# Performance work log

Measured on AMD Instinct MI355X. Metric: run time of the kernel, lower is better.

Reference implementation:

```python
import jax, jax.numpy as jnp
import numpy as np

MAX_SEQ = 512
HIDDEN = 1024
E = 2 * HIDDEN  # expansion
S = 128         # head dim s
EPS = 1e-5


def setup_inputs() -> dict:
    key = jax.random.key(0)
    ks = jax.random.split(key, 10)
    B, N = 32, 512
    x = jax.random.normal(ks[0], (B, N, HIDDEN), dtype=jnp.float32)
    attention_mask = jnp.ones((B, N), dtype=jnp.float32)
    gamma = jax.random.uniform(ks[1], (2, S), dtype=jnp.float32)
    beta = jax.random.uniform(ks[2], (2, S), dtype=jnp.float32)
    w = jax.random.uniform(ks[3], (2 * MAX_SEQ - 1,), dtype=jnp.float32)
    a_p = jax.random.uniform(ks[4], (1, S), dtype=jnp.float32)
    b_p = jax.random.uniform(ks[5], (1, S), dtype=jnp.float32)
    # uv: Linear(hidden -> 2e+s), stored input-major for x @ uv_w
    uv_w = jax.random.normal(ks[6], (HIDDEN, 2 * E + S), dtype=jnp.float32) * 0.02
    uv_b = jnp.zeros((2 * E + S,), dtype=jnp.float32)
    o_w = jax.random.normal(ks[7], (E, HIDDEN), dtype=jnp.float32) * 0.02
    o_b = jnp.zeros((HIDDEN,), dtype=jnp.float32)
    ln_g = jnp.ones((HIDDEN,), dtype=jnp.float32)
    ln_b = jnp.zeros((HIDDEN,), dtype=jnp.float32)
    return {"x": x, "attention_mask": attention_mask, "gamma": gamma, "beta": beta,
            "w": w, "a_p": a_p, "b_p": b_p, "uv_w": uv_w, "uv_b": uv_b,
            "o_w": o_w, "o_b": o_b, "ln_g": ln_g, "ln_b": ln_b}


def _rope_seq(x):
    # x: [b, n, 2, s]; rotary positions along axis 1 (matches module's rope(x, dim=1))
    n, d = x.shape[1], x.shape[-1]
    half = d // 2
    pos = jnp.arange(n, dtype=jnp.float32)
    # inv_freq = 10000 ** (arange(half)/half)  (freq_seq = -arange/half, inv = 10000**-freq_seq)
    inv_freq = jnp.power(10000.0, jnp.arange(half, dtype=jnp.float32) / half)
    sinusoid = pos[:, None] * inv_freq  # [n, half]
    sin = jnp.sin(sinusoid)[None, :, None, :]
    cos = jnp.cos(sinusoid)[None, :, None, :]
    x1, x2 = jnp.split(x, 2, axis=-1)
    return jnp.concatenate([x1 * cos - x2 * sin, x2 * cos + x1 * sin], axis=-1)


def _rel_pos_bias(w, seq_len):
    # Toeplitz trick (max_seq_length <= 512 path)
    t = jnp.pad(w[: 2 * MAX_SEQ - 1], (0, MAX_SEQ))          # [3S-1]
    t = jnp.tile(t, MAX_SEQ)[: -MAX_SEQ].reshape(-1, MAX_SEQ, 3 * MAX_SEQ - 2)
    r = (2 * MAX_SEQ - 1) // 2
    t = t[..., r:-r]                                          # [1, S, S]
    return t[:, :seq_len, :seq_len]


def reference(x, attention_mask, gamma, beta, w, a_p, b_p, uv_w, uv_b, o_w, o_b, ln_g, ln_b):
    n = x.shape[1]
    shortcut = x
    mu = jnp.mean(x, axis=-1, keepdims=True)
    var = jnp.mean(jnp.square(x - mu), axis=-1, keepdims=True)
    xn = (x - mu) * jax.lax.rsqrt(var + EPS) * ln_g + ln_b
    uv = jax.nn.silu(xn @ uv_w + uv_b)                        # [b, n, 2e+s]
    u, v, base = jnp.split(uv, [E, 2 * E], axis=-1)
    base = base[..., None, :] * gamma + beta                  # [b, n, 2, s]
    base = _rope_seq(base)
    q, k = base[:, :, 0], base[:, :, 1]                       # [b, n, s]
    qk = jnp.einsum('bnd,bmd->bnm', q, k)
    qk = qk + ((1.0 - attention_mask) * -1e12)[:, None, :]
    bias = _rel_pos_bias(w, n)                                # [1, n, n]
    kernel = jnp.square(jax.nn.relu(qk / MAX_SEQ + bias))
    out = u * jnp.einsum('bnm,bme->bne', kernel, v)           # [b, n, e]
    return out @ o_w + o_b + shortcut
```

## Files before the change

kernel.cpp:

```cpp
#include <hip/hip_runtime.h>
#include <math.h>

#define HIDDEN 1024
#define NSEQ   512
#define BATCH  32
#define EDIM   2048
#define SDIM   128
#define UVN    (2 * EDIM + SDIM)

using short8  = __attribute__((ext_vector_type(8))) short;
using float4x = __attribute__((ext_vector_type(4))) float;

__device__ __forceinline__ ushort f2bf(float f) {
    unsigned u = __float_as_uint(f);
    u += 0x7FFFu + ((u >> 16) & 1u);
    return (ushort)(u >> 16);
}
__device__ __forceinline__ float bf2f(ushort h) {
    return __uint_as_float(((unsigned)h) << 16);
}

#define ASYNC16(gp, lp) __builtin_amdgcn_global_load_lds( \
    (const __attribute__((address_space(1))) unsigned int*)(unsigned long long)(const void*)(gp), \
    (__attribute__((address_space(3))) unsigned int*)(unsigned int)(unsigned long long)(const void*)(lp), \
    16, 0, 0)

__global__ __launch_bounds__(64) void tab_kernel(float* __restrict__ sin_t,
                                                 float* __restrict__ cos_t) {
    int i = blockIdx.x;
    int j = threadIdx.x;
    double inv = pow(10000.0, (double)j / 64.0);
    double ang = (double)i * inv;
    sin_t[i * 64 + j] = (float)sin(ang);
    cos_t[i * 64 + j] = (float)cos(ang);
}

__global__ __launch_bounds__(256) void transpose_f32_bf16(const float* __restrict__ src,
                                                          ushort* __restrict__ dst,
                                                          int R, int Cc) {
    __shared__ float tile[32][33];
    const int bx = blockIdx.x;
    const int by = blockIdx.y;
    const int lx = threadIdx.x & 31;
    const int gy = threadIdx.x >> 5;
#pragma unroll
    for (int i = 0; i < 4; ++i) {
        int r = by * 32 + gy + i * 8;
        tile[gy + i * 8][lx] = src[(size_t)r * Cc + bx * 32 + lx];
    }
    __syncthreads();
#pragma unroll
    for (int i = 0; i < 4; ++i) {
        int c = bx * 32 + gy + i * 8;
        dst[(size_t)c * R + by * 32 + lx] = f2bf(tile[lx][gy + i * 8]);
    }
}

__global__ __launch_bounds__(256) void ln_kernel(const float* __restrict__ x,
                                                 const float* __restrict__ g,
                                                 const float* __restrict__ b,
                                                 ushort* __restrict__ xn) {
    const size_t t = blockIdx.x;
    const int tid = threadIdx.x;
    const float4 v = ((const float4*)(x + t * HIDDEN))[tid];
    float s = v.x + v.y + v.z + v.w;
#pragma unroll
    for (int off = 32; off > 0; off >>= 1) s += __shfl_down(s, off);
    __shared__ float red[4];
    const int wid = tid >> 6, lane = tid & 63;
    if (lane == 0) red[wid] = s;
    __syncthreads();
    const float mean = (red[0] + red[1] + red[2] + red[3]) * (1.0f / HIDDEN);
    __syncthreads();
    const float dx = v.x - mean, dy = v.y - mean, dz = v.z - mean, dw = v.w - mean;
    float s2 = dx * dx + dy * dy + dz * dz + dw * dw;
#pragma unroll
    for (int off = 32; off > 0; off >>= 1) s2 += __shfl_down(s2, off);
    if (lane == 0) red[wid] = s2;
    __syncthreads();
    const float var = (red[0] + red[1] + red[2] + red[3]) * (1.0f / HIDDEN);
    const float rs = rsqrtf(var + 1e-5f);
    const float4 gv = ((const float4*)g)[tid];
    const float4 bv = ((const float4*)b)[tid];
    ushort4 o;
    o.x = f2bf(dx * rs * gv.x + bv.x);
    o.y = f2bf(dy * rs * gv.y + bv.y);
    o.z = f2bf(dz * rs * gv.z + bv.z);
    o.w = f2bf(dw * rs * gv.w + bv.w);
    ((ushort4*)(xn + t * HIDDEN))[tid] = o;
}

__device__ __forceinline__ void mfma_core_128(const ushort* __restrict__ A,
                                              const ushort* __restrict__ Bt,
                                              const int lda, const int ldb, const int K,
                                              const int m0, const int n0,
                                              ushort* As, ushort* Bs,
                                              float4x (&acc)[4][4]) {
    const int tid = threadIdx.x;
    const int l = tid & 63, w = tid >> 6;
    const int wm = (w & 1) << 6, wn = (w >> 1) << 6;

    const int c0 = w * 128 + l;
    const int r0 = c0 >> 2, kc0 = (c0 & 3) * 8;
    const int c1 = c0 + 64;
    const int r1 = c1 >> 2, kc1 = (c1 & 3) * 8;
    char* ldsA0 = (char*)As + (size_t)(w * 128) * 16;
    char* ldsA1 = ldsA0 + 1024;
    char* ldsB0 = (char*)Bs + (size_t)(w * 128) * 16;
    char* ldsB1 = ldsB0 + 1024;
    const ushort* gA0 = A + (size_t)(m0 + r0) * lda + kc0;
    const ushort* gA1 = A + (size_t)(m0 + r1) * lda + kc1;
    const ushort* gB0 = Bt + (size_t)(n0 + r0) * ldb + kc0;
    const ushort* gB1 = Bt + (size_t)(n0 + r1) * ldb + kc1;

    const int lr = l & 15, lk = (l >> 4) * 8;
    int aoff[4], boff[4];
#pragma unroll
    for (int i = 0; i < 4; ++i) {
        aoff[i] = (wm + i * 16 + lr) * 32 + lk;
        boff[i] = (wn + i * 16 + lr) * 32 + lk;
    }

    for (int k0 = 0; k0 < K; k0 += 32) {
        __syncthreads();
        ASYNC16(gA0 + k0, ldsA0);
        ASYNC16(gA1 + k0, ldsA1);
        ASYNC16(gB0 + k0, ldsB0);
        ASYNC16(gB1 + k0, ldsB1);
        __syncthreads();
        short8 af[4], bfr[4];
#pragma unroll
        for (int i = 0; i < 4; ++i) af[i] = *(const short8*)(As + aoff[i]);
#pragma unroll
        for (int i = 0; i < 4; ++i) bfr[i] = *(const short8*)(Bs + boff[i]);
#pragma unroll
        for (int mi = 0; mi < 4; ++mi)
#pragma unroll
            for (int ni = 0; ni < 4; ++ni)
                acc[mi][ni] = __builtin_amdgcn_mfma_f32_16x16x32_bf16(
                    af[mi], bfr[ni], acc[mi][ni], 0, 0, 0);
    }
}

template <typename F>
__device__ __forceinline__ void epilogue_loop(const float4x (&acc)[4][4],
                                              int m0, int n0, F body) {
    const int l = threadIdx.x & 63, w = threadIdx.x >> 6;
    const int wm = (w & 1) << 6, wn = (w >> 1) << 6;
    const int lrow = (l >> 4) << 2, lcol = l & 15;
#pragma unroll
    for (int mi = 0; mi < 4; ++mi)
#pragma unroll
        for (int ni = 0; ni < 4; ++ni)
#pragma unroll
            for (int r = 0; r < 4; ++r) {
                const int m = m0 + wm + mi * 16 + lrow + r;
                const int n = n0 + wn + ni * 16 + lcol;
                body(m, n, acc[mi][ni][r]);
            }
}

__device__ __forceinline__ void mfma_core_256(const ushort* __restrict__ A,
                                              const ushort* __restrict__ Bt,
                                              const int lda, const int ldb, const int K,
                                              const int m0, const int n0,
                                              char* smem,
                                              float4x (&acc)[8][4]) {
    const int tid = threadIdx.x;
    const int l = tid & 63, w = tid >> 6;
    const int wm = w >> 2, wn = w & 3;

    const int srow = l >> 2;
    const int kcol = (w & 1) * 32 + (((tid & 3) ^ ((l >> 3) & 3)) << 3);
    const int rb0  = w >> 1;
    const ushort* gA[4];
    const ushort* gB[4];
#pragma unroll
    for (int j = 0; j < 4; ++j) {
        const int row = (j * 4 + rb0) * 16 + srow;
        gA[j] = A  + (size_t)(m0 + row) * lda + kcol;
        gB[j] = Bt + (size_t)(n0 + row) * ldb + kcol;
    }
    char* const ldsA = smem;
    char* const ldsB = smem + 65536;
    const int wdst = w * 1024;

#define STG_A(buf, j, t)  ASYNC16(gA[j] + (size_t)(t) * 64, ldsA + (buf) * 32768 + (j) * 8192 + wdst)
#define STG_B(buf, j, t)  ASYNC16(gB[j] + (size_t)(t) * 64, ldsB + (buf) * 32768 + (j) * 8192 + wdst)
#define RAWBAR() do { __builtin_amdgcn_sched_barrier(0); __builtin_amdgcn_s_barrier(); \
                      __builtin_amdgcn_sched_barrier(0); } while (0)

    const int LB = (l & 15) * 64 + (((l >> 4) ^ ((l >> 1) & 3)) << 4);
    const int rbbA0 = wm * 4;
    const int rbbA1 = 8 + wm * 4;
    const int cbbB0 = wn * 2;
    const int cbbB1 = 8 + wn * 2;

    const int KT = K >> 6;

    STG_A(0, 0, 0); STG_A(0, 1, 0); STG_A(0, 2, 0); STG_A(0, 3, 0);
    STG_B(0, 0, 0); STG_B(0, 1, 0); STG_B(0, 2, 0); STG_B(0, 3, 0);
    STG_A(1, 0, 1); STG_A(1, 1, 1); STG_B(1, 2, 1); STG_B(1, 3, 1);
    asm volatile("s_waitcnt vmcnt(4)" ::: "memory");
    RAWBAR();

    for (int t = 0; t < KT; ++t) {
        const int buf = t & 1, nbuf = buf ^ 1;
        const char* Ab = ldsA + buf * 32768;
        const char* Bb = ldsB + buf * 32768;
        short8 a[4][2], bb[2][2];

#pragma unroll
        for (int mi = 0; mi < 4; ++mi) {
            a[mi][0] = *(const short8*)(Ab + (rbbA0 + mi) * 2048 + LB);
            a[mi][1] = *(const short8*)(Ab + (rbbA0 + mi) * 2048 + 1024 + LB);
        }
#pragma unroll
        for (int ni = 0; ni < 2; ++ni) {
            bb[ni][0] = *(const short8*)(Bb + (cbbB0 + ni) * 2048 + LB);
            bb[ni][1] = *(const short8*)(Bb + (cbbB0 + ni) * 2048 + 1024 + LB);
        }
        if (t + 1 < KT) { STG_A(nbuf, 2, t + 1); STG_A(nbuf, 3, t + 1); }
        RAWBAR();
        __builtin_amdgcn_s_setprio(1);
#pragma unroll
        for (int mi = 0; mi < 4; ++mi)
#pragma unroll
            for (int ni = 0; ni < 2; ++ni) {
                acc[mi][ni] = __builtin_amdgcn_mfma_f32_16x16x32_bf16(a[mi][0], bb[ni][0], acc[mi][ni], 0, 0, 0);
                acc[mi][ni] = __builtin_amdgcn_mfma_f32_16x16x32_bf16(a[mi][1], bb[ni][1], acc[mi][ni], 0, 0, 0);
            }
        __builtin_amdgcn_s_setprio(0);
        RAWBAR();

#pragma unroll
        for (int ni = 0; ni < 2; ++ni) {
            bb[ni][0] = *(const short8*)(Bb + (cbbB1 + ni) * 2048 + LB);
            bb[ni][1] = *(const short8*)(Bb + (cbbB1 + ni) * 2048 + 1024 + LB);
        }
        if (t + 1 < KT) { STG_B(nbuf, 0, t + 1); STG_B(nbuf, 1, t + 1); }
        RAWBAR();
        __builtin_amdgcn_s_setprio(1);
#pragma unroll
        for (int mi = 0; mi < 4; ++mi)
#pragma unroll
            for (int ni = 0; ni < 2; ++ni) {
                acc[mi][2 + ni] = __builtin_amdgcn_mfma_f32_16x16x32_bf16(a[mi][0], bb[ni][0], acc[mi][2 + ni], 0, 0, 0);
                acc[mi][2 + ni] = __builtin_amdgcn_mfma_f32_16x16x32_bf16(a[mi][1], bb[ni][1], acc[mi][2 + ni], 0, 0, 0);
            }
        __builtin_amdgcn_s_setprio(0);
        RAWBAR();

#pragma unroll
        for (int mi = 0; mi < 4; ++mi) {
            a[mi][0] = *(const short8*)(Ab + (rbbA1 + mi) * 2048 + LB);
            a[mi][1] = *(const short8*)(Ab + (rbbA1 + mi) * 2048 + 1024 + LB);
        }
        if (t + 2 < KT) { STG_A(buf, 0, t + 2); STG_A(buf, 1, t + 2); }
        RAWBAR();
        __builtin_amdgcn_s_setprio(1);
#pragma unroll
        for (int mi = 0; mi < 4; ++mi)
#pragma unroll
            for (int ni = 0; ni < 2; ++ni) {
                acc[4 + mi][2 + ni] = __builtin_amdgcn_mfma_f32_16x16x32_bf16(a[mi][0], bb[ni][0], acc[4 + mi][2 + ni], 0, 0, 0);
                acc[4 + mi][2 + ni] = __builtin_amdgcn_mfma_f32_16x16x32_bf16(a[mi][1], bb[ni][1], acc[4 + mi][2 + ni], 0, 0, 0);
            }
        __builtin_amdgcn_s_setprio(0);
        RAWBAR();

#pragma unroll
        for (int ni = 0; ni < 2; ++ni) {
            bb[ni][0] = *(const short8*)(Bb + (cbbB0 + ni) * 2048 + LB);
            bb[ni][1] = *(const short8*)(Bb + (cbbB0 + ni) * 2048 + 1024 + LB);
        }
        if (t + 2 < KT) { STG_B(buf, 2, t + 2); STG_B(buf, 3, t + 2); }
        __builtin_amdgcn_sched_barrier(0);
        __builtin_amdgcn_s_setprio(1);
#pragma unroll
        for (int mi = 0; mi < 4; ++mi)
#pragma unroll
            for (int ni = 0; ni < 2; ++ni) {
                acc[4 + mi][ni] = __builtin_amdgcn_mfma_f32_16x16x32_bf16(a[mi][0], bb[ni][0], acc[4 + mi][ni], 0, 0, 0);
                acc[4 + mi][ni] = __builtin_amdgcn_mfma_f32_16x16x32_bf16(a[mi][1], bb[ni][1], acc[4 + mi][ni], 0, 0, 0);
            }
        __builtin_amdgcn_s_setprio(0);
        if (t + 2 < KT) asm volatile("s_waitcnt vmcnt(4)" ::: "memory");
        else            asm volatile("s_waitcnt vmcnt(0)" ::: "memory");
        RAWBAR();
    }
#undef STG_A
#undef STG_B
#undef RAWBAR
}

template <typename F>
__device__ __forceinline__ void epilogue_256(const float4x (&acc)[8][4],
                                             int m0, int n0, F body) {
    const int tid = threadIdx.x;
    const int l = tid & 63, w = tid >> 6;
    const int wm = w >> 2, wn = w & 3;
    const int lrow = (l >> 4) << 2, lcol = l & 15;
#pragma unroll
    for (int i = 0; i < 8; ++i)
#pragma unroll
        for (int j = 0; j < 4; ++j)
#pragma unroll
            for (int r = 0; r < 4; ++r) {
                const int m = m0 + (i >> 2) * 128 + wm * 64 + (i & 3) * 16 + lrow + r;
                const int n = n0 + (j >> 1) * 128 + wn * 32 + (j & 1) * 16 + lcol;
                body(m, n, acc[i][j][r]);
            }
}

__global__ __launch_bounds__(512) void gemm_uv2(const ushort* __restrict__ A,
                                                const ushort* __restrict__ Bt,
                                                const float* __restrict__ bias,
                                                ushort* __restrict__ U,
                                                ushort* __restrict__ VT) {
    __shared__ __align__(16) char smem[131072];
    float4x acc[8][4] = {};
    const int n0 = blockIdx.x * 256, m0 = blockIdx.y * 256;
    mfma_core_256(A, Bt, HIDDEN, HIDDEN, HIDDEN, m0, n0, smem, acc);
    if (blockIdx.x < 8) {
        epilogue_256(acc, m0, n0, [&](int m, int n, float aval) {
            float val = aval + bias[n];
            val = val / (1.0f + expf(-val));
            U[(size_t)m * EDIM + n] = f2bf(val);
        });
    } else {
        epilogue_256(acc, m0, n0, [&](int m, int n, float aval) {
            float val = aval + bias[n];
            val = val / (1.0f + expf(-val));
            const int e = n - EDIM;
            const int b = m >> 9;
            const int s = m & (NSEQ - 1);
            VT[((size_t)b * EDIM + e) * NSEQ + s] = f2bf(val);
        });
    }
}

__global__ __launch_bounds__(256) void gemm_base_mfma(const ushort* __restrict__ A,
                                                      const ushort* __restrict__ Bt,
                                                      const float* __restrict__ bias,
                                                      float* __restrict__ BASE) {
    __shared__ ushort As[128 * 32], Bs[128 * 32];
    float4x acc[4][4] = {};
    const int n0 = 2 * EDIM;
    const int m0 = blockIdx.y * 128;
    mfma_core_128(A, Bt, HIDDEN, HIDDEN, HIDDEN, m0, n0, As, Bs, acc);
    epilogue_loop(acc, m0, n0, [&](int m, int n, float aval) {
        float val = aval + bias[n];
        val = val / (1.0f + expf(-val));
        BASE[(size_t)m * SDIM + (n - 2 * EDIM)] = val;
    });
}

__global__ __launch_bounds__(128) void rope_kernel(const float* __restrict__ base,
                                                   const float* __restrict__ gamma,
                                                   const float* __restrict__ beta,
                                                   const float* __restrict__ sin_t,
                                                   const float* __restrict__ cos_t,
                                                   float* __restrict__ q,
                                                   float* __restrict__ k) {
    const size_t t = blockIdx.x;
    const int d = threadIdx.x;
    const int pos = (int)(t & (NSEQ - 1));
    __shared__ float vq[128], vk[128];
    const float bval = base[t * SDIM + d];
    vq[d] = bval * gamma[d] + beta[d];
    vk[d] = bval * gamma[SDIM + d] + beta[SDIM + d];
    __syncthreads();
    const int h = d & 63;
    const float sn = sin_t[pos * 64 + h];
    const float cs = cos_t[pos * 64 + h];
    float oq, ok;
    if (d < 64) {
        oq = vq[d] * cs - vq[d + 64] * sn;
        ok = vk[d] * cs - vk[d + 64] * sn;
    } else {
        oq = vq[d] * cs + vq[d - 64] * sn;
        ok = vk[d] * cs + vk[d - 64] * sn;
    }
    q[t * SDIM + d] = oq;
    k[t * SDIM + d] = ok;
}

__global__ __launch_bounds__(256) void gemm_qk(const float* __restrict__ q,
                                               const float* __restrict__ k,
                                               const float* __restrict__ mask,
                                               const float* __restrict__ w,
                                               ushort* __restrict__ km) {
    __shared__ float As[16][68];
    __shared__ float Bs[16][68];
    const int b = blockIdx.z;
    const float* A = q + (size_t)b * NSEQ * SDIM;
    const float* B = k + (size_t)b * NSEQ * SDIM;
    const int tid = threadIdx.x;
    const int tx = tid & 15, ty = tid >> 4;
    const int arow = tid >> 2, acol = (tid & 3) << 2;
    const int n0 = blockIdx.x * 64, m0 = blockIdx.y * 64;
    float acc[4][4] = {};
    for (int k0 = 0; k0 < SDIM; k0 += 16) {
        float4 av = *(const float4*)(A + (size_t)(m0 + arow) * SDIM + (k0 + acol));
        float4 bv = *(const float4*)(B + (size_t)(n0 + arow) * SDIM + (k0 + acol));
        As[acol + 0][arow] = av.x; As[acol + 1][arow] = av.y;
        As[acol + 2][arow] = av.z; As[acol + 3][arow] = av.w;
        Bs[acol + 0][arow] = bv.x; Bs[acol + 1][arow] = bv.y;
        Bs[acol + 2][arow] = bv.z; Bs[acol + 3][arow] = bv.w;
        __syncthreads();
#pragma unroll
        for (int kk = 0; kk < 16; ++kk) {
            const float4 a4 = *(const float4*)&As[kk][ty << 2];
            const float4 b4 = *(const float4*)&Bs[kk][tx << 2];
            const float a[4] = {a4.x, a4.y, a4.z, a4.w};
            const float bbv[4] = {b4.x, b4.y, b4.z, b4.w};
#pragma unroll
            for (int i = 0; i < 4; ++i)
#pragma unroll
                for (int j = 0; j < 4; ++j)
                    acc[i][j] = fmaf(a[i], bbv[j], acc[i][j]);
        }
        __syncthreads();
    }
    const float inv512 = 1.0f / 512.0f;
#pragma unroll
    for (int i = 0; i < 4; ++i) {
        const int ii = m0 + (ty << 2) + i;
#pragma unroll
        for (int j = 0; j < 4; ++j) {
            const int jj = n0 + (tx << 2) + j;
            const float mterm = (1.0f - mask[b * NSEQ + jj]) * -1e12f;
            float val = (acc[i][j] + mterm) * inv512 + w[511 + jj - ii];
            val = fmaxf(val, 0.0f);
            km[(size_t)b * NSEQ * NSEQ + (size_t)ii * NSEQ + jj] = f2bf(val * val);
        }
    }
}

__global__ __launch_bounds__(512) void gemm_pv2(const ushort* __restrict__ km,
                                                const ushort* __restrict__ vT,
                                                ushort* __restrict__ ug) {
    __shared__ __align__(16) char smem[131072];
    float4x acc[8][4] = {};
    const int b = blockIdx.z;
    const int n0 = blockIdx.x * 256, m0 = blockIdx.y * 256;
    mfma_core_256(km + (size_t)b * NSEQ * NSEQ, vT + (size_t)b * EDIM * NSEQ,
                  NSEQ, NSEQ, NSEQ, m0, n0, smem, acc);
    const size_t tokbase = (size_t)b * NSEQ;
    epilogue_256(acc, m0, n0, [&](int m, int n, float aval) {
        const size_t idx = (tokbase + m) * EDIM + n;
        ug[idx] = f2bf(bf2f(ug[idx]) * aval);
    });
}

__global__ __launch_bounds__(512) void gemm_out2(const ushort* __restrict__ A,
                                                 const ushort* __restrict__ Bt,
                                                 const float* __restrict__ ob,
                                                 const float* __restrict__ x,
                                                 float* __restrict__ out) {
    __shared__ __align__(16) char smem[131072];
    float4x acc[8][4] = {};
    const int n0 = blockIdx.x * 256, m0 = blockIdx.y * 256;
    mfma_core_256(A, Bt, EDIM, EDIM, EDIM, m0, n0, smem, acc);
    epilogue_256(acc, m0, n0, [&](int m, int n, float aval) {
        out[(size_t)m * HIDDEN + n] = aval + ob[n] + x[(size_t)m * HIDDEN + n];
    });
}

extern "C" void kernel_launch(void* const* d_in, const int* in_sizes, int n_in,
                              void* d_out, int out_size, void* d_ws, size_t ws_size,
                              hipStream_t stream) {
    const float* x     = (const float*)d_in[0];
    const float* mask  = (const float*)d_in[1];
    const float* gamma = (const float*)d_in[2];
    const float* beta  = (const float*)d_in[3];
    const float* w     = (const float*)d_in[4];
    const float* uv_w  = (const float*)d_in[7];
    const float* uv_b  = (const float*)d_in[8];
    const float* o_w   = (const float*)d_in[9];
    const float* o_b   = (const float*)d_in[10];
    const float* ln_g  = (const float*)d_in[11];
    const float* ln_b  = (const float*)d_in[12];
    float* out = (float*)d_out;

    int C = 32;
    while (C > 1) {
        unsigned long long need = (unsigned long long)C * 5505024ull + 13107200ull;
        if (need <= (unsigned long long)ws_size) break;
        C >>= 1;
    }
    const int R = C * NSEQ;

    char* p = (char*)d_ws;
    ushort* xn  = (ushort*)p;  p += (size_t)C * 1048576;
    ushort* u   = (ushort*)p;  p += (size_t)C * 2097152;
    ushort* vT  = (ushort*)p;  p += (size_t)C * 2097152;
    float* base = (float*)p;   p += (size_t)C * 262144;
    float* sint = (float*)p;   p += 131072;
    float* cost = (float*)p;   p += 131072;
    ushort* uv_wt = (ushort*)p; p += 8650752;
    ushort* o_wt  = (ushort*)p; p += 4194304;
    float* q  = (float*)xn;
    float* k  = (float*)((char*)xn + (size_t)C * 262144);
    ushort* km = (ushort*)((char*)xn + (size_t)C * 524288);

    hipLaunchKernelGGL(tab_kernel, dim3(512), dim3(64), 0, stream, sint, cost);
    hipLaunchKernelGGL(transpose_f32_bf16, dim3(132, 32), dim3(256), 0, stream,
                       uv_w, uv_wt, HIDDEN, UVN);
    hipLaunchKernelGGL(transpose_f32_bf16, dim3(32, 64), dim3(256), 0, stream,
                       o_w, o_wt, EDIM, HIDDEN);

    for (int b0 = 0; b0 < BATCH; b0 += C) {
        const float* xc = x + (size_t)b0 * NSEQ * HIDDEN;
        float*       oc = out + (size_t)b0 * NSEQ * HIDDEN;
        const float* mc = mask + (size_t)b0 * NSEQ;
        hipLaunchKernelGGL(ln_kernel, dim3(R), dim3(256), 0, stream, xc, ln_g, ln_b, xn);
        hipLaunchKernelGGL(gemm_uv2, dim3(16, R / 256), dim3(512), 0, stream,
                           xn, uv_wt, uv_b, u, vT);
        hipLaunchKernelGGL(gemm_base_mfma, dim3(1, R / 128), dim3(256), 0, stream,
                           xn, uv_wt, uv_b, base);
        hipLaunchKernelGGL(rope_kernel, dim3(R), dim3(128), 0, stream,
                           base, gamma, beta, sint, cost, q, k);
        hipLaunchKernelGGL(gemm_qk, dim3(8, 8, C), dim3(256), 0, stream, q, k, mc, w, km);
        hipLaunchKernelGGL(gemm_pv2, dim3(8, 2, C), dim3(512), 0, stream, km, vT, u);
        hipLaunchKernelGGL(gemm_out2, dim3(4, R / 256), dim3(512), 0, stream,
                           u, o_wt, o_b, xc, oc);
    }
}
```

Before: 556.7 us.

## Restructure GEMM main loop into three phases with deeper B prefetch

Reworks the 256x256 bf16 MFMA GEMM main loop. It keeps separate register copies of both B column halves, so the last quadrant reuses the first B fragments instead of reloading them from LDS, which removes one LDS read round and one barrier per k-step. The async global-to-LDS stores are rescheduled so that all of the next-next B tile is issued in one phase. Finer vmcnt waits keep more loads in flight. The change adds register pressure and relies on hand-tuned vmcnt counts, which could be wrong at the tail iterations.

```diff
diff --git a/kernel.cpp b/kernel.cpp
--- a/kernel.cpp
+++ b/kernel.cpp
@@ -189,6 +189,7 @@
 #define STG_B(buf, j, t)  ASYNC16(gB[j] + (size_t)(t) * 64, ldsB + (buf) * 32768 + (j) * 8192 + wdst)
 #define RAWBAR() do { __builtin_amdgcn_sched_barrier(0); __builtin_amdgcn_s_barrier(); \
                       __builtin_amdgcn_sched_barrier(0); } while (0)
+#define WAITV(N) asm volatile("s_waitcnt vmcnt(" #N ")" ::: "memory")
 
     const int LB = (l & 15) * 64 + (((l >> 4) ^ ((l >> 1) & 3)) << 4);
     const int rbbA0 = wm * 4;
@@ -198,17 +199,21 @@
 
     const int KT = K >> 6;
 
-    STG_A(0, 0, 0); STG_A(0, 1, 0); STG_A(0, 2, 0); STG_A(0, 3, 0);
-    STG_B(0, 0, 0); STG_B(0, 1, 0); STG_B(0, 2, 0); STG_B(0, 3, 0);
-    STG_A(1, 0, 1); STG_A(1, 1, 1); STG_B(1, 2, 1); STG_B(1, 3, 1);
-    asm volatile("s_waitcnt vmcnt(4)" ::: "memory");
+    STG_A(0, 0, 0); STG_A(0, 1, 0);
+    STG_B(0, 0, 0); STG_B(0, 1, 0);
+    STG_B(0, 2, 0); STG_B(0, 3, 0);
+    STG_A(0, 2, 0); STG_A(0, 3, 0);
+    STG_A(1, 0, 1); STG_A(1, 1, 1);
+    STG_B(1, 0, 1); STG_B(1, 1, 1);
+    STG_B(1, 2, 1); STG_B(1, 3, 1);
+    WAITV(10);
     RAWBAR();
 
     for (int t = 0; t < KT; ++t) {
         const int buf = t & 1, nbuf = buf ^ 1;
         const char* Ab = ldsA + buf * 32768;
         const char* Bb = ldsB + buf * 32768;
-        short8 a[4][2], bb[2][2];
+        short8 a[4][2], b0[2][2], b1[2][2];
 
 #pragma unroll
         for (int mi = 0; mi < 4; ++mi) {
@@ -217,8 +222,8 @@
         }
 #pragma unroll
         for (int ni = 0; ni < 2; ++ni) {
-            bb[ni][0] = *(const short8*)(Bb + (cbbB0 + ni) * 2048 + LB);
-            bb[ni][1] = *(const short8*)(Bb + (cbbB0 + ni) * 2048 + 1024 + LB);
+            b0[ni][0] = *(const short8*)(Bb + (cbbB0 + ni) * 2048 + LB);
+            b0[ni][1] = *(const short8*)(Bb + (cbbB0 + ni) * 2048 + 1024 + LB);
         }
         if (t + 1 < KT) { STG_A(nbuf, 2, t + 1); STG_A(nbuf, 3, t + 1); }
         RAWBAR();
@@ -227,28 +232,30 @@
         for (int mi = 0; mi < 4; ++mi)
 #pragma unroll
             for (int ni = 0; ni < 2; ++ni) {
-                acc[mi][ni] = __builtin_amdgcn_mfma_f32_16x16x32_bf16(a[mi][0], bb[ni][0], acc[mi][ni], 0, 0, 0);
-                acc[mi][ni] = __builtin_amdgcn_mfma_f32_16x16x32_bf16(a[mi][1], bb[ni][1], acc[mi][ni], 0, 0, 0);
+                acc[mi][ni] = __builtin_amdgcn_mfma_f32_16x16x32_bf16(a[mi][0], b0[ni][0], acc[mi][ni], 0, 0, 0);
+                acc[mi][ni] = __builtin_amdgcn_mfma_f32_16x16x32_bf16(a[mi][1], b0[ni][1], acc[mi][ni], 0, 0, 0);
             }
         __builtin_amdgcn_s_setprio(0);
+        if (t < KT - 1) { WAITV(10); } else { WAITV(2); }
         RAWBAR();
 
 #pragma unroll
         for (int ni = 0; ni < 2; ++ni) {
-            bb[ni][0] = *(const short8*)(Bb + (cbbB1 + ni) * 2048 + LB);
-            bb[ni][1] = *(const short8*)(Bb + (cbbB1 + ni) * 2048 + 1024 + LB);
-        }
-        if (t + 1 < KT) { STG_B(nbuf, 0, t + 1); STG_B(nbuf, 1, t + 1); }
+            b1[ni][0] = *(const short8*)(Bb + (cbbB1 + ni) * 2048 + LB);
+            b1[ni][1] = *(const short8*)(Bb + (cbbB1 + ni) * 2048 + 1024 + LB);
+        }
+        if (t + 2 < KT) { STG_A(buf, 0, t + 2); STG_A(buf, 1, t + 2); }
         RAWBAR();
         __builtin_amdgcn_s_setprio(1);
 #pragma unroll
         for (int mi = 0; mi < 4; ++mi)
 #pragma unroll
             for (int ni = 0; ni < 2; ++ni) {
-                acc[mi][2 + ni] = __builtin_amdgcn_mfma_f32_16x16x32_bf16(a[mi][0], bb[ni][0], acc[mi][2 + ni], 0, 0, 0);
-                acc[mi][2 + ni] = __builtin_amdgcn_mfma_f32_16x16x32_bf16(a[mi][1], bb[ni][1], acc[mi][2 + ni], 0, 0, 0);
+                acc[mi][2 + ni] = __builtin_amdgcn_mfma_f32_16x16x32_bf16(a[mi][0], b1[ni][0], acc[mi][2 + ni], 0, 0, 0);
+                acc[mi][2 + ni] = __builtin_amdgcn_mfma_f32_16x16x32_bf16(a[mi][1], b1[ni][1], acc[mi][2 + ni], 0, 0, 0);
             }
         __builtin_amdgcn_s_setprio(0);
+        if (t < KT - 2) { WAITV(10); } else if (t == KT - 2) { WAITV(8); } else { WAITV(0); }
         RAWBAR();
 
 #pragma unroll
@@ -256,42 +263,34 @@
             a[mi][0] = *(const short8*)(Ab + (rbbA1 + mi) * 2048 + LB);
             a[mi][1] = *(const short8*)(Ab + (rbbA1 + mi) * 2048 + 1024 + LB);
         }
-        if (t + 2 < KT) { STG_A(buf, 0, t + 2); STG_A(buf, 1, t + 2); }
+        if (t + 2 < KT) {
+            STG_B(buf, 0, t + 2); STG_B(buf, 1, t + 2);
+            STG_B(buf, 2, t + 2); STG_B(buf, 3, t + 2);
+        }
         RAWBAR();
         __builtin_amdgcn_s_setprio(1);
 #pragma unroll
         for (int mi = 0; mi < 4; ++mi)
 #pragma unroll
             for (int ni = 0; ni < 2; ++ni) {
-                acc[4 + mi][2 + ni] = __builtin_amdgcn_mfma_f32_16x16x32_bf16(a[mi][0], bb[ni][0], acc[4 + mi][2 + ni], 0, 0, 0);
-                acc[4 + mi][2 + ni] = __builtin_amdgcn_mfma_f32_16x16x32_bf16(a[mi][1], bb[ni][1], acc[4 + mi][2 + ni], 0, 0, 0);
+                acc[4 + mi][2 + ni] = __builtin_amdgcn_mfma_f32_16x16x32_bf16(a[mi][0], b1[ni][0], acc[4 + mi][2 + ni], 0, 0, 0);
+                acc[4 + mi][2 + ni] = __builtin_amdgcn_mfma_f32_16x16x32_bf16(a[mi][1], b1[ni][1], acc[4 + mi][2 + ni], 0, 0, 0);
+            }
+#pragma unroll
+        for (int mi = 0; mi < 4; ++mi)
+#pragma unroll
+            for (int ni = 0; ni < 2; ++ni) {
+                acc[4 + mi][ni] = __builtin_amdgcn_mfma_f32_16x16x32_bf16(a[mi][0], b0[ni][0], acc[4 + mi][ni], 0, 0, 0);
+                acc[4 + mi][ni] = __builtin_amdgcn_mfma_f32_16x16x32_bf16(a[mi][1], b0[ni][1], acc[4 + mi][ni], 0, 0, 0);
             }
         __builtin_amdgcn_s_setprio(0);
-        RAWBAR();
-
-#pragma unroll
-        for (int ni = 0; ni < 2; ++ni) {
-            bb[ni][0] = *(const short8*)(Bb + (cbbB0 + ni) * 2048 + LB);
-            bb[ni][1] = *(const short8*)(Bb + (cbbB0 + ni) * 2048 + 1024 + LB);
-        }
-        if (t + 2 < KT) { STG_B(buf, 2, t + 2); STG_B(buf, 3, t + 2); }
-        __builtin_amdgcn_sched_barrier(0);
-        __builtin_amdgcn_s_setprio(1);
-#pragma unroll
-        for (int mi = 0; mi < 4; ++mi)
-#pragma unroll
-            for (int ni = 0; ni < 2; ++ni) {
-                acc[4 + mi][ni] = __builtin_amdgcn_mfma_f32_16x16x32_bf16(a[mi][0], bb[ni][0], acc[4 + mi][ni], 0, 0, 0);
-                acc[4 + mi][ni] = __builtin_amdgcn_mfma_f32_16x16x32_bf16(a[mi][1], bb[ni][1], acc[4 + mi][ni], 0, 0, 0);
-            }
-        __builtin_amdgcn_s_setprio(0);
-        if (t + 2 < KT) asm volatile("s_waitcnt vmcnt(4)" ::: "memory");
-        else            asm volatile("s_waitcnt vmcnt(0)" ::: "memory");
+        if (t < KT - 2) { WAITV(10); } else if (t == KT - 2) { WAITV(4); }
         RAWBAR();
     }
 #undef STG_A
 #undef STG_B
 #undef RAWBAR
+#undef WAITV
 }
 
 template <typename F>
```

Result: no change. 550.4 us (-1.1%).
